# Kernel optimization log

Measured on AMD Instinct MI355X. Metric: run time of the kernel, lower is better.

Reference implementation:

```python
import jax, jax.numpy as jnp
import numpy as np

BIG = 1e10  # penalty for cross-batch pairs in masked knn


def knn_interpolate(x, pos, pos_skip, batch, batch_skip, k):
    # squared pairwise distances [N_skip, N] via ||a||^2 + ||b||^2 - 2 a.b (avoids [Ns,N,3] temp)
    d2 = (jnp.sum(pos_skip**2, -1)[:, None]
          + jnp.sum(pos**2, -1)[None, :]
          - 2.0 * (pos_skip @ pos.T))
    d2 = jnp.maximum(d2, 0.0)
    # mask out neighbors from a different cloud in the batch
    d2 = d2 + jnp.where(batch_skip[:, None] != batch[None, :], BIG, 0.0)
    neg_d2k, idx = jax.lax.top_k(-d2, k)          # k smallest distances
    d2k = -neg_d2k                                # [N_skip, k]
    w = 1.0 / jnp.clip(d2k, 1e-16)                # inverse squared-distance weights (PyG convention)
    xk = x[idx]                                   # gather neighbor features [N_skip, k, C]
    return jnp.sum(w[..., None] * xk, axis=1) / jnp.sum(w, axis=1, keepdims=True)


def setup_inputs() -> dict:
    key = jax.random.key(0)
    ks = jax.random.split(key, 8)
    B, N, Ns, C, Cs, H = 4, 4096, 16384, 256, 128, 512
    x = jax.random.normal(ks[0], (N, C), dtype=jnp.float32)
    pos = jax.random.normal(ks[1], (N, 3), dtype=jnp.float32)
    batch = jnp.repeat(jnp.arange(B, dtype=jnp.int64), N // B)
    x_skip = jax.random.normal(ks[2], (Ns, Cs), dtype=jnp.float32)
    pos_skip = jax.random.normal(ks[3], (Ns, 3), dtype=jnp.float32)
    batch_skip = jnp.repeat(jnp.arange(B, dtype=jnp.int64), Ns // B)
    fan_in1, fan_in2 = C + Cs, H
    W1 = jax.random.normal(ks[4], (fan_in1, H), dtype=jnp.float32) / np.sqrt(fan_in1)
    b1 = jnp.zeros((H,), dtype=jnp.float32)
    W2 = jax.random.normal(ks[5], (H, H), dtype=jnp.float32) / np.sqrt(fan_in2)
    b2 = jnp.zeros((H,), dtype=jnp.float32)
    return {"x": x, "pos": pos, "batch": batch, "x_skip": x_skip,
            "pos_skip": pos_skip, "batch_skip": batch_skip,
            "W1": W1, "b1": b1, "W2": W2, "b2": b2, "k": 3}


def reference(x, pos, batch, x_skip, pos_skip, batch_skip, W1, b1, W2, b2, k):
    xi = knn_interpolate(x, pos, pos_skip, batch, batch_skip, k)  # [Ns, C]
    h = jnp.concatenate([xi, x_skip], axis=1)                     # [Ns, C+Cs]
    h = jax.nn.relu(h @ W1 + b1)
    h = jax.nn.relu(h @ W2 + b2)
    return (h, pos_skip, batch_skip)
```

## Files before the change

kernel.cpp:

```cpp
#include <hip/hip_runtime.h>
#include <hip/hip_bf16.h>
#include <float.h>


#define KNN_K 3
#define NBATCH 4

typedef __attribute__((ext_vector_type(8))) __bf16 bf16x8;
typedef __attribute__((ext_vector_type(4))) __bf16 bf16x4;
typedef __attribute__((ext_vector_type(4))) float  f32x4;
typedef unsigned long long ull;

__device__ __forceinline__ void gload_lds16(const void* g, void* l) {
    __builtin_amdgcn_global_load_lds(
        (const __attribute__((address_space(1))) unsigned int*)g,
        (__attribute__((address_space(3))) unsigned int*)l, 16, 0, 0);
}

template<int K>
__device__ __forceinline__ void insK(ull (&key)[K], ull c) {
    if (c < key[K-1]) {
        key[K-1] = c;
#pragma unroll
        for (int p = K-1; p >= 1; --p) {
            if (key[p] < key[p-1]) {
                ull t = key[p-1]; key[p-1] = key[p]; key[p] = t;
            }
        }
    }
}

template<int SPAN, int C, int Cs>
__global__ __launch_bounds__(256) void knn_wprep_fast(
    const float* __restrict__ x, const float* __restrict__ pos,
    const int* __restrict__ batch, const float* __restrict__ x_skip,
    const float* __restrict__ pos_skip, const int* __restrict__ batch_skip,
    __bf16* __restrict__ h0, float* __restrict__ out_tail, int Ns,
    const float* __restrict__ W1, const float* __restrict__ W2,
    __bf16* __restrict__ W1t, __bf16* __restrict__ W2t,
    int K1, int H, int H2, int knnBlocks)
{
    __shared__ float4 pos4[SPAN];
    __shared__ ull    skey[256 * KNN_K];
    __shared__ int    sidx[16][KNN_K];
    __shared__ float  swt [16][KNN_K + 1];
    __shared__ float  Ws[32][33];

    const int t = threadIdx.x;

    if (blockIdx.x >= knnBlocks) {
        int b = blockIdx.x - knnBlocks;
        const float* W; __bf16* Wt; int kt, nt, K, Ncols;
        const int nt1 = H / 32, n1 = (K1 / 32) * nt1;
        if (b < n1) { W = W1; Wt = W1t; K = K1; Ncols = H;  kt = b / nt1; nt = b % nt1; }
        else { b -= n1; const int nt2 = H2 / 32;
               W = W2; Wt = W2t; K = H;  Ncols = H2; kt = b / nt2; nt = b % nt2; }
        const int r = t >> 5, c = t & 31;
#pragma unroll
        for (int i = 0; i < 4; ++i)
            Ws[r + i*8][c] = W[(size_t)(kt*32 + r + i*8) * Ncols + nt*32 + c];
        __syncthreads();
#pragma unroll
        for (int i = 0; i < 4; ++i)
            Wt[(size_t)(nt*32 + r + i*8) * K + kt*32 + c] = (__bf16)Ws[c][r + i*8];
        return;
    }

    const int q0 = blockIdx.x * 16;
    const int bs    = batch_skip[q0];
    const int cbase = bs * SPAN;

    for (int i = t; i < SPAN; i += 256) {
        const int j = cbase + i;
        const float qx = pos[j*3+0], qy = pos[j*3+1], qz = pos[j*3+2];
        float pn2 = qx*qx + qy*qy + qz*qz;
        if (batch[j] != bs) pn2 = 3.0e38f;
        pos4[i] = make_float4(qx, qy, qz, pn2);
    }

    if (t < 48)               out_tail[q0*3 + t] = pos_skip[q0*3 + t];
    else if (t < 64)          out_tail[(size_t)Ns*3 + q0 + (t-48)] =
                                  (float)batch_skip[q0 + (t-48)];
    __syncthreads();

    const int q   = t & 15;
    const int g   = t >> 4;
    const int qq  = q0 + q;
    const float px = pos_skip[qq*3+0], py = pos_skip[qq*3+1], pz = pos_skip[qq*3+2];
    const float ps2 = px*px + py*py + pz*pz;

    ull kA[KNN_K], kB[KNN_K], kC[KNN_K], kD[KNN_K];
#pragma unroll
    for (int j = 0; j < KNN_K; ++j) { kA[j]=~0ull; kB[j]=~0ull; kC[j]=~0ull; kD[j]=~0ull; }

    const int base = g * (SPAN / 16);
#pragma unroll 4
    for (int i = 0; i < 16; ++i) {
        const int ii = (i + g) & 15;
        const int jA = base + ii;
        const int jB = base + 16 + ii;
        const int jC = base + 32 + ii;
        const int jD = base + 48 + ii;
        const float4 pA = pos4[jA];
        const float4 pB = pos4[jB];
        const float4 pC = pos4[jC];
        const float4 pD = pos4[jD];
        float d2A = (ps2 + pA.w) - 2.0f*(px*pA.x + py*pA.y + pz*pA.z);
        float d2B = (ps2 + pB.w) - 2.0f*(px*pB.x + py*pB.y + pz*pB.z);
        float d2C = (ps2 + pC.w) - 2.0f*(px*pC.x + py*pC.y + pz*pC.z);
        float d2D = (ps2 + pD.w) - 2.0f*(px*pD.x + py*pD.y + pz*pD.z);
        d2A = fmaxf(d2A, 0.0f); d2B = fmaxf(d2B, 0.0f);
        d2C = fmaxf(d2C, 0.0f); d2D = fmaxf(d2D, 0.0f);
        insK<KNN_K>(kA, ((ull)__float_as_uint(d2A) << 32) | (unsigned)(cbase + jA));
        insK<KNN_K>(kB, ((ull)__float_as_uint(d2B) << 32) | (unsigned)(cbase + jB));
        insK<KNN_K>(kC, ((ull)__float_as_uint(d2C) << 32) | (unsigned)(cbase + jC));
        insK<KNN_K>(kD, ((ull)__float_as_uint(d2D) << 32) | (unsigned)(cbase + jD));
    }
#pragma unroll
    for (int j = 0; j < KNN_K; ++j) insK<KNN_K>(kA, kB[j]);
#pragma unroll
    for (int j = 0; j < KNN_K; ++j) insK<KNN_K>(kA, kC[j]);
#pragma unroll
    for (int j = 0; j < KNN_K; ++j) insK<KNN_K>(kA, kD[j]);

#pragma unroll
    for (int j = 0; j < KNN_K; ++j) skey[t*KNN_K + j] = kA[j];
    __syncthreads();

    if (t < 16) {
        ull key[KNN_K];
#pragma unroll
        for (int j = 0; j < KNN_K; ++j) key[j] = skey[t*KNN_K + j];
#pragma unroll
        for (int gg = 1; gg < 16; ++gg)
#pragma unroll
            for (int j = 0; j < KNN_K; ++j)
                insK<KNN_K>(key, skey[(t + 16*gg)*KNN_K + j]);
        float wv[KNN_K]; float wsum = 0.0f;
#pragma unroll
        for (int j = 0; j < KNN_K; ++j) {
            const float d2 = __uint_as_float((unsigned)(key[j] >> 32));
            sidx[t][j] = (int)(key[j] & 0xFFFFFFFFull);
            wv[j] = 1.0f / fmaxf(d2, 1e-16f);
            wsum += wv[j];
            swt[t][j] = wv[j];
        }
        swt[t][KNN_K] = 1.0f / wsum;
    }
    __syncthreads();

    {
        const int gq  = t >> 4;
        const int sub = t & 15;
        const int s   = q0 + gq;
        const int i0 = sidx[gq][0], i1 = sidx[gq][1], i2 = sidx[gq][2];
        const float w0 = swt[gq][0], w1 = swt[gq][1], w2 = swt[gq][2];
        const float inv = swt[gq][3];
        __bf16* hrow = h0 + (size_t)s * (C + Cs);
        const float* x0 = &x[(size_t)i0*C];
        const float* x1 = &x[(size_t)i1*C];
        const float* x2 = &x[(size_t)i2*C];

#pragma unroll
        for (int cc = 0; cc < C; cc += 64) {
            const int c = cc + sub*4;
            const float4 v0 = *(const float4*)&x0[c];
            const float4 v1 = *(const float4*)&x1[c];
            const float4 v2 = *(const float4*)&x2[c];
            bf16x4 o;
            o[0] = (__bf16)((w0*v0.x + w1*v1.x + w2*v2.x) * inv);
            o[1] = (__bf16)((w0*v0.y + w1*v1.y + w2*v2.y) * inv);
            o[2] = (__bf16)((w0*v0.z + w1*v1.z + w2*v2.z) * inv);
            o[3] = (__bf16)((w0*v0.w + w1*v1.w + w2*v2.w) * inv);
            *(bf16x4*)&hrow[c] = o;
        }
#pragma unroll
        for (int cc = 0; cc < Cs; cc += 64) {
            const int c = cc + sub*4;
            const float4 v = *(const float4*)&x_skip[(size_t)s*Cs + c];
            bf16x4 o;
            o[0] = (__bf16)v.x; o[1] = (__bf16)v.y;
            o[2] = (__bf16)v.z; o[3] = (__bf16)v.w;
            *(bf16x4*)&hrow[C + c] = o;
        }
    }
}

__global__ __launch_bounds__(512) void knn_concat_kernel(
    const float* __restrict__ x, const float* __restrict__ pos,
    const int* __restrict__ batch, const float* __restrict__ x_skip,
    const float* __restrict__ pos_skip, const int* __restrict__ batch_skip,
    __bf16* __restrict__ h0, float* __restrict__ out_tail,
    int N, int C, int Cs, int Ns)
{
    const int t    = threadIdx.x;
    const int lane = t & 63;
    const int wav  = t >> 6;
    const int q0   = blockIdx.x * 64;
    const int q    = q0 + lane;

    __shared__ float4 pos4[1024];
    __shared__ ull    skey[512 * KNN_K];
    __shared__ int    sidx[64][KNN_K];
    __shared__ float  swt [64][KNN_K + 1];

    const int span  = N / NBATCH;
    const int bs    = batch_skip[q0];
    const int cbase = bs * span;

    for (int i = t; i < span; i += 512) {
        const int j = cbase + i;
        const float qx = pos[j*3+0], qy = pos[j*3+1], qz = pos[j*3+2];
        float pn2 = qx*qx + qy*qy + qz*qz;
        if (batch[j] != bs) pn2 = 3.0e38f;
        pos4[i] = make_float4(qx, qy, qz, pn2);
    }
    if (t < 192)              out_tail[q0*3 + t] = pos_skip[q0*3 + t];
    else if (t < 256)         out_tail[(size_t)Ns*3 + q0 + (t-192)] =
                                  (float)batch_skip[q0 + (t-192)];
    __syncthreads();

    const float px = pos_skip[q*3+0], py = pos_skip[q*3+1], pz = pos_skip[q*3+2];
    const float ps2 = px*px + py*py + pz*pz;

    ull key[KNN_K];
#pragma unroll
    for (int j = 0; j < KNN_K; ++j) key[j] = ~0ull;

    const int chunk = span / 8;
    const int c0    = wav * chunk;
#pragma unroll 4
    for (int i = 0; i < chunk; ++i) {
        const int jj = c0 + i;
        const float4 p = pos4[jj];
        const float dot = px*p.x + py*p.y + pz*p.z;
        float d2 = (ps2 + p.w) - 2.0f*dot;
        d2 = fmaxf(d2, 0.0f);
        insK<KNN_K>(key, ((ull)__float_as_uint(d2) << 32) | (unsigned)(cbase + jj));
    }
#pragma unroll
    for (int j = 0; j < KNN_K; ++j) skey[t*KNN_K + j] = key[j];
    __syncthreads();

    if (t < 64) {
#pragma unroll
        for (int ww = 1; ww < 8; ++ww)
#pragma unroll
            for (int j = 0; j < KNN_K; ++j)
                insK<KNN_K>(key, skey[(t + 64*ww)*KNN_K + j]);
        float wv[KNN_K]; float wsum = 0.0f;
#pragma unroll
        for (int j = 0; j < KNN_K; ++j) {
            const float d2 = __uint_as_float((unsigned)(key[j] >> 32));
            sidx[t][j] = (int)(key[j] & 0xFFFFFFFFull);
            wv[j] = 1.0f / fmaxf(d2, 1e-16f);
            wsum += wv[j];
            swt[t][j] = wv[j];
        }
        swt[t][KNN_K] = 1.0f / wsum;
    }
    __syncthreads();

    {
        const int gq  = t >> 3;
        const int sub = t & 7;
        const int s   = q0 + gq;
        const int i0 = sidx[gq][0], i1 = sidx[gq][1], i2 = sidx[gq][2];
        const float w0 = swt[gq][0], w1 = swt[gq][1], w2 = swt[gq][2];
        const float inv = swt[gq][3];
        __bf16* hrow = h0 + (size_t)s * (C + Cs);

        for (int c = sub*4; c < C; c += 32) {
            const float4 v0 = *(const float4*)&x[(size_t)i0*C + c];
            const float4 v1 = *(const float4*)&x[(size_t)i1*C + c];
            const float4 v2 = *(const float4*)&x[(size_t)i2*C + c];
            bf16x4 o;
            o[0] = (__bf16)((w0*v0.x + w1*v1.x + w2*v2.x) * inv);
            o[1] = (__bf16)((w0*v0.y + w1*v1.y + w2*v2.y) * inv);
            o[2] = (__bf16)((w0*v0.z + w1*v1.z + w2*v2.z) * inv);
            o[3] = (__bf16)((w0*v0.w + w1*v1.w + w2*v2.w) * inv);
            *(bf16x4*)&hrow[c] = o;
        }
        for (int c = sub*4; c < Cs; c += 32) {
            const float4 v = *(const float4*)&x_skip[(size_t)s*Cs + c];
            bf16x4 o;
            o[0] = (__bf16)v.x; o[1] = (__bf16)v.y;
            o[2] = (__bf16)v.z; o[3] = (__bf16)v.w;
            *(bf16x4*)&hrow[C + c] = o;
        }
    }
}

__global__ __launch_bounds__(256) void wprep_kernel(
    const float* __restrict__ W1, const float* __restrict__ W2,
    __bf16* __restrict__ W1t, __bf16* __restrict__ W2t,
    int K1, int H, int H2)
{
    __shared__ float Ws[32][33];
    int b = blockIdx.x;
    const float* W; __bf16* Wt; int kt, nt, K, Ncols;
    const int nt1 = H / 32, n1 = (K1 / 32) * nt1;
    if (b < n1) { W = W1; Wt = W1t; K = K1; Ncols = H;  kt = b / nt1; nt = b % nt1; }
    else { b -= n1; const int nt2 = H2 / 32;
           W = W2; Wt = W2t; K = H;  Ncols = H2; kt = b / nt2; nt = b % nt2; }

    const int t = threadIdx.x;
    const int r = t >> 5, c = t & 31;
#pragma unroll
    for (int i = 0; i < 4; ++i)
        Ws[r + i*8][c] = W[(size_t)(kt*32 + r + i*8) * Ncols + nt*32 + c];
    __syncthreads();
#pragma unroll
    for (int i = 0; i < 4; ++i)
        Wt[(size_t)(nt*32 + r + i*8) * K + kt*32 + c] = (__bf16)Ws[c][r + i*8];
}

template<bool OUT_BF16>
__global__ __launch_bounds__(256) void gemm_mfma(
    const __bf16* __restrict__ A, const __bf16* __restrict__ Bt,
    const float* __restrict__ bias, void* __restrict__ Cout,
    int M, int N, int K)
{
    const int BK = 64;
    __shared__ __bf16 As[128 * BK];
    __shared__ __bf16 Bs[128 * BK];

    const int t    = threadIdx.x;
    const int wave = t >> 6, lane = t & 63;
    const int row0 = blockIdx.y * 128;
    const int col0 = blockIdx.x * 128;
    const int wr   = (wave >> 1) * 64;
    const int wc   = (wave & 1)  * 64;

    const int lr = lane & 15;
    const int lk = (lane >> 4) * 8;

    f32x4 acc[4][4] = {};

    for (int k0 = 0; k0 < K; k0 += BK) {
#pragma unroll
        for (int i = 0; i < 4; ++i) {
            const int ebase = (i*4 + wave) * 512;
            const int e = ebase + lane*8;
            const int r = e >> 6, c = e & 63;
            gload_lds16(&A[(size_t)(row0 + r)*K + k0 + c], &As[ebase]);
        }
#pragma unroll
        for (int i = 0; i < 4; ++i) {
            const int ebase = (i*4 + wave) * 512;
            const int e = ebase + lane*8;
            const int r = e >> 6, c = e & 63;
            gload_lds16(&Bt[(size_t)(col0 + r)*K + k0 + c], &Bs[ebase]);
        }
        __syncthreads();

#pragma unroll
        for (int kk = 0; kk < BK; kk += 32) {
            bf16x8 a[4], b[4];
#pragma unroll
            for (int m = 0; m < 4; ++m)
                a[m] = *(const bf16x8*)&As[(wr + m*16 + lr)*BK + kk + lk];
#pragma unroll
            for (int n = 0; n < 4; ++n)
                b[n] = *(const bf16x8*)&Bs[(wc + n*16 + lr)*BK + kk + lk];
#pragma unroll
            for (int m = 0; m < 4; ++m)
#pragma unroll
                for (int n = 0; n < 4; ++n)
                    acc[m][n] = __builtin_amdgcn_mfma_f32_16x16x32_bf16(
                        a[m], b[n], acc[m][n], 0, 0, 0);
        }
        __syncthreads();
    }

    const int orow = (lane >> 4) * 4;
#pragma unroll
    for (int m = 0; m < 4; ++m) {
#pragma unroll
        for (int n = 0; n < 4; ++n) {
            const int ccol = col0 + wc + n*16 + lr;
            const float bv = bias[ccol];
#pragma unroll
            for (int j = 0; j < 4; ++j) {
                const int crow = row0 + wr + m*16 + orow + j;
                const float v = fmaxf(acc[m][n][j] + bv, 0.0f);
                if (OUT_BF16) ((__bf16*)Cout)[(size_t)crow*N + ccol] = (__bf16)v;
                else          ((float*)Cout)[(size_t)crow*N + ccol]  = v;
            }
        }
    }
}

extern "C" void kernel_launch(void* const* d_in, const int* in_sizes, int n_in,
                              void* d_out, int out_size, void* d_ws, size_t ws_size,
                              hipStream_t stream)
{
    const float* x          = (const float*)d_in[0];
    const float* pos        = (const float*)d_in[1];
    const int*   batch      = (const int*)  d_in[2];
    const float* x_skip     = (const float*)d_in[3];
    const float* pos_skip   = (const float*)d_in[4];
    const int*   batch_skip = (const int*)  d_in[5];
    const float* W1         = (const float*)d_in[6];
    const float* b1         = (const float*)d_in[7];
    const float* W2         = (const float*)d_in[8];
    const float* b2         = (const float*)d_in[9];

    const int N  = in_sizes[2];
    const int Ns = in_sizes[5];
    const int C  = in_sizes[0] / N;
    const int Cs = in_sizes[3] / Ns;
    const int H  = in_sizes[7];
    const int H2 = in_sizes[9];
    const int K1 = C + Cs;

    __bf16* h0  = (__bf16*)d_ws;
    __bf16* h1  = h0  + (size_t)Ns * K1;
    __bf16* W1t = h1  + (size_t)Ns * H;
    __bf16* W2t = W1t + (size_t)H  * K1;
    float*  out = (float*)d_out;

    const int nblk_w = (K1 / 32) * (H / 32) + (H / 32) * (H2 / 32);

    if (N == 4096 && C == 256 && Cs == 128) {
        const int knnBlocks = Ns / 16;
        knn_wprep_fast<1024, 256, 128><<<knnBlocks + nblk_w, 256, 0, stream>>>(
            x, pos, batch, x_skip, pos_skip, batch_skip, h0,
            out + (size_t)Ns * H2, Ns,
            W1, W2, W1t, W2t, K1, H, H2, knnBlocks);
    } else {
        knn_concat_kernel<<<Ns / 64, 512, 0, stream>>>(
            x, pos, batch, x_skip, pos_skip, batch_skip, h0,
            out + (size_t)Ns * H2, N, C, Cs, Ns);
        wprep_kernel<<<nblk_w, 256, 0, stream>>>(W1, W2, W1t, W2t, K1, H, H2);
    }

    dim3 g1(H  / 128, Ns / 128);
    gemm_mfma<true ><<<g1, 256, 0, stream>>>(h0, W1t, b1, (void*)h1, Ns, H,  K1);

    dim3 g2(H2 / 128, Ns / 128);
    gemm_mfma<false><<<g2, 256, 0, stream>>>(h1, W2t, b2, (void*)out, Ns, H2, H);
}
```

Measured before the change: 58.41 us.

## Add full-K A-staged GEMM with direct global B loads for fast path

Adds a GEMM kernel that stages a 64-row A tile covering the whole K dimension in swizzled LDS in one pass. It then streams B fragments directly from global memory, so the loop has no k-loop barriers. The grid is ordered with row blocks first, so that neighbouring blocks share weight columns in cache. Both MLP layers on the fast path use it, and the old 128x128 LDS-tiled GEMM stays as the fallback. The trade-off is that B reads now rely on L2 instead of LDS reuse, and the large LDS allocation (up to 64KB) may lower occupancy.

Result: slower. 102.6 us (+75.6%).

```diff
diff --git a/kernel.cpp b/kernel.cpp
--- a/kernel.cpp
+++ b/kernel.cpp
@@ -186,6 +186,73 @@
     }
 }
 
+template<int K, bool OUT_BF16>
+__global__ __launch_bounds__(256) void gemm_astage(
+    const __bf16* __restrict__ A,
+    const __bf16* __restrict__ Bt,
+    const float* __restrict__ bias,
+    void* __restrict__ Cout,
+    int M, int N)
+{
+    __shared__ __bf16 As[64 * K];
+
+    const int t    = threadIdx.x;
+    const int wave = t >> 6, lane = t & 63;
+    const int row0 = blockIdx.x * 64;
+    const int col0 = blockIdx.y * 128;
+    const int wr   = (wave >> 1) * 32;
+    const int wc   = (wave & 1)  * 64;
+    const int lr   = lane & 15;
+    const int lk   = (lane >> 4) * 8;
+
+    const int CPR = K / 8;
+    for (int c = t; c < 64 * CPR; c += 256) {
+        const int r = c / CPR, kc = c - r * CPR;
+        const bf16x8 v = *(const bf16x8*)&A[(size_t)(row0 + r)*K + kc*8];
+        const int byte = ((r*K + kc*8) * 2) ^ ((r & 7) << 4);
+        *(bf16x8*)((char*)As + byte) = v;
+    }
+    __syncthreads();
+
+    f32x4 acc[2][4] = {};
+#pragma unroll
+    for (int kk = 0; kk < K; kk += 32) {
+        bf16x8 a[2], b[4];
+#pragma unroll
+        for (int m = 0; m < 2; ++m) {
+            const int r = wr + m*16 + lr;
+            const int byte = ((r*K + kk + lk) * 2) ^ ((r & 7) << 4);
+            a[m] = *(const bf16x8*)((const char*)As + byte);
+        }
+#pragma unroll
+        for (int n = 0; n < 4; ++n)
+            b[n] = *(const bf16x8*)&Bt[(size_t)(col0 + wc + n*16 + lr)*K + kk + lk];
+#pragma unroll
+        for (int m = 0; m < 2; ++m)
+#pragma unroll
+            for (int n = 0; n < 4; ++n)
+                acc[m][n] = __builtin_amdgcn_mfma_f32_16x16x32_bf16(
+                    a[m], b[n], acc[m][n], 0, 0, 0);
+    }
+
+    const int orow = (lane >> 4) * 4;
+#pragma unroll
+    for (int m = 0; m < 2; ++m) {
+#pragma unroll
+        for (int n = 0; n < 4; ++n) {
+            const int ccol = col0 + wc + n*16 + lr;
+            const float bv = bias[ccol];
+#pragma unroll
+            for (int j = 0; j < 4; ++j) {
+                const int crow = row0 + wr + m*16 + orow + j;
+                const float v = fmaxf(acc[m][n][j] + bv, 0.0f);
+                if (OUT_BF16) ((__bf16*)Cout)[(size_t)crow*N + ccol] = (__bf16)v;
+                else          ((float*)Cout)[(size_t)crow*N + ccol]  = v;
+            }
+        }
+    }
+}
+
 __global__ __launch_bounds__(512) void knn_concat_kernel(
     const float* __restrict__ x, const float* __restrict__ pos,
     const int* __restrict__ batch, const float* __restrict__ x_skip,
@@ -331,7 +398,6 @@
     const int col0 = blockIdx.x * 128;
     const int wr   = (wave >> 1) * 64;
     const int wc   = (wave & 1)  * 64;
-
     const int lr = lane & 15;
     const int lk = (lane >> 4) * 8;
 
@@ -421,23 +487,30 @@
     float*  out = (float*)d_out;
 
     const int nblk_w = (K1 / 32) * (H / 32) + (H / 32) * (H2 / 32);
-
-    if (N == 4096 && C == 256 && Cs == 128) {
+    const bool fast = (N == 4096 && C == 256 && Cs == 128 &&
+                       H == 512 && H2 == 512 && (Ns % 64) == 0);
+
+    if (fast) {
         const int knnBlocks = Ns / 16;
         knn_wprep_fast<1024, 256, 128><<<knnBlocks + nblk_w, 256, 0, stream>>>(
             x, pos, batch, x_skip, pos_skip, batch_skip, h0,
             out + (size_t)Ns * H2, Ns,
             W1, W2, W1t, W2t, K1, H, H2, knnBlocks);
+
+        dim3 g1(Ns / 64, H / 128);
+        gemm_astage<384, true ><<<g1, 256, 0, stream>>>(h0, W1t, b1, (void*)h1, Ns, H);
+
+        dim3 g2(Ns / 64, H2 / 128);
+        gemm_astage<512, false><<<g2, 256, 0, stream>>>(h1, W2t, b2, (void*)out, Ns, H2);
     } else {
         knn_concat_kernel<<<Ns / 64, 512, 0, stream>>>(
             x, pos, batch, x_skip, pos_skip, batch_skip, h0,
             out + (size_t)Ns * H2, N, C, Cs, Ns);
         wprep_kernel<<<nblk_w, 256, 0, stream>>>(W1, W2, W1t, W2t, K1, H, H2);
-    }
-
-    dim3 g1(H  / 128, Ns / 128);
-    gemm_mfma<true ><<<g1, 256, 0, stream>>>(h0, W1t, b1, (void*)h1, Ns, H,  K1);
-
-    dim3 g2(H2 / 128, Ns / 128);
-    gemm_mfma<false><<<g2, 256, 0, stream>>>(h1, W2t, b2, (void*)out, Ns, H2, H);
-}
+
+        dim3 g1(H / 128, Ns / 128);
+        gemm_mfma<true ><<<g1, 256, 0, stream>>>(h0, W1t, b1, (void*)h1, Ns, H,  K1);
+        dim3 g2(H2 / 128, Ns / 128);
+        gemm_mfma<false><<<g2, 256, 0, stream>>>(h1, W2t, b2, (void*)out, Ns, H2, H);
+    }
+}
```
